# Performance work log

Hardware: AMD Instinct MI355X
Metric: run time of the kernel (lower is better)

The kernel has to match this reference:

```python
import jax, jax.numpy as jnp
import numpy as np
import math

D_MODEL = 2048
NUM_HEADS = 16
D_K = D_MODEL // NUM_HEADS  # 128
THETA = 10000.0
BATCH = 2
SEQ = 2048


def setup_inputs() -> dict:
    key = jax.random.key(0)
    k1, k2, k3 = jax.random.split(key, 3)
    std_qkv = math.sqrt(2.0 / (D_MODEL + 3 * D_MODEL))
    std_o = math.sqrt(2.0 / (D_MODEL + D_MODEL))
    return {
        "x": jax.random.normal(k1, (BATCH, SEQ, D_MODEL), dtype=jnp.float32),
        "token_positions": jnp.arange(SEQ, dtype=jnp.int64 if jax.config.jax_enable_x64 else jnp.int32),
        "Wqkv": jax.random.normal(k2, (3 * D_MODEL, D_MODEL), dtype=jnp.float32) * std_qkv,
        "Wo": jax.random.normal(k3, (D_MODEL, D_MODEL), dtype=jnp.float32) * std_o,
    }


def _rope(x, positions):
    # x: [b, h, t, d_k]; interleaved even/odd rotation as in the torch module
    half = D_K // 2
    inv_freq = 1.0 / (THETA ** (jnp.arange(half, dtype=x.dtype) / half))
    ang = positions.astype(x.dtype)[:, None] * inv_freq[None, :]  # [t, half]
    sin, cos = jnp.sin(ang), jnp.cos(ang)                          # broadcast over b,h
    x_even, x_odd = x[..., 0::2], x[..., 1::2]
    rot_even = x_even * cos - x_odd * sin
    rot_odd = x_even * sin + x_odd * cos
    return jnp.stack([rot_even, rot_odd], axis=-1).reshape(x.shape)


def reference(x, token_positions, Wqkv, Wo):
    B, T, _ = x.shape
    qkv = x @ Wqkv.T                                  # [b, t, 3*d_model]
    q, k, v = jnp.split(qkv, 3, axis=-1)
    def to_heads(t):
        return t.reshape(B, T, NUM_HEADS, D_K).transpose(0, 2, 1, 3)  # b h t d
    q, k, v = to_heads(q), to_heads(k), to_heads(v)
    q = _rope(q, token_positions)
    k = _rope(k, token_positions)
    scale = 1.0 / math.sqrt(D_K)
    scores = jnp.einsum("bhqd,bhkd->bhqk", q, k) * scale
    causal = jnp.tril(jnp.ones((T, T), dtype=bool))
    scores = jnp.where(causal, scores, jnp.finfo(scores.dtype).min)
    attn = jax.nn.softmax(scores, axis=-1)
    out = jnp.einsum("bhqk,bhkd->bhqd", attn, v)
    out = out.transpose(0, 2, 1, 3).reshape(B, T, D_MODEL)
    return out @ Wo.T
```

## Files before the change

### kernel.cpp

```cpp
#include <hip/hip_runtime.h>
#include <math.h>
#include <stdint.h>

#define NHEADS 16
#define DK 128
#define TSEQ 2048
#define DMODEL 2048

typedef __attribute__((ext_vector_type(8))) short short8;
typedef __attribute__((ext_vector_type(4))) float floatx4;

__device__ __forceinline__ float bf2f(unsigned short h) {
    return __uint_as_float(((unsigned int)h) << 16);
}
__device__ __forceinline__ unsigned short f2bf(float f) {
    unsigned int u = __float_as_uint(f);
    u += 0x7FFFu + ((u >> 16) & 1u);
    return (unsigned short)(u >> 16);
}
__device__ __forceinline__ void async16(unsigned short* lds, const unsigned short* g) {
    __builtin_amdgcn_global_load_lds(
        (const __attribute__((address_space(1))) uint32_t*)g,
        (__attribute__((address_space(3))) uint32_t*)lds, 16, 0, 0);
}

#define NX8 1048576
#define NW8 1572864
#define NO8 524288
__global__ __launch_bounds__(256) void cast_all_bf16(
    const float* __restrict__ x, const float* __restrict__ wqkv, const float* __restrict__ wo,
    unsigned short* __restrict__ xb, unsigned short* __restrict__ wqkvb, unsigned short* __restrict__ wob)
{
    const int i = blockIdx.x * 256 + threadIdx.x;
    const float* src; unsigned short* dst; int k;
    if (i < NX8)            { src = x;    dst = xb;    k = i; }
    else if (i < NX8 + NW8) { src = wqkv; dst = wqkvb; k = i - NX8; }
    else                    { src = wo;   dst = wob;   k = i - NX8 - NW8; }
    const float4* p4 = reinterpret_cast<const float4*>(src) + 2 * (size_t)k;
    const float4 a = p4[0], b = p4[1];
    uint32_t w0 = (uint32_t)f2bf(a.x) | ((uint32_t)f2bf(a.y) << 16);
    uint32_t w1 = (uint32_t)f2bf(a.z) | ((uint32_t)f2bf(a.w) << 16);
    uint32_t w2 = (uint32_t)f2bf(b.x) | ((uint32_t)f2bf(b.y) << 16);
    uint32_t w3 = (uint32_t)f2bf(b.z) | ((uint32_t)f2bf(b.w) << 16);
    uint4 o; o.x = w0; o.y = w1; o.z = w2; o.w = w3;
    *reinterpret_cast<uint4*>(dst + 8 * (size_t)k) = o;
}

__global__ __launch_bounds__(256) void rope_table_kernel(
    const int* __restrict__ pos, float2* __restrict__ tab)
{
    const int idx = blockIdx.x * 256 + threadIdx.x;
    const int tt = idx >> 6, i = idx & 63;
    const double inv_freq = exp(-log(10000.0) * (double)i / 64.0);
    const double ang = (double)pos[tt] * inv_freq;
    tab[idx] = make_float2((float)cos(ang), (float)sin(ang));
}

__global__ __launch_bounds__(512, 1) void gemm_qkv_8ph(
    const unsigned short* __restrict__ A, const unsigned short* __restrict__ B,
    unsigned short* __restrict__ qkvb, unsigned short* __restrict__ vt,
    const float2* __restrict__ tab)
{
    const int K = DMODEL, N = 3 * DMODEL;
    __shared__ unsigned short As[2][256 * 64];
    __shared__ unsigned short Bs[2][192 * 64];

    const int t = threadIdx.x;
    const int lane = t & 63, w = t >> 6;
    const int wr = w >> 2, wc = w & 3;
    const int lr = lane & 15, hi = lane >> 4;

    const int bid = (int)blockIdx.x;
    const int xcd = bid & 7, local = bid >> 3;
    const int row0 = (local & 15) * 256;
    const int col0 = ((xcd << 2) | (local >> 4)) * 192;

    const int rr = t >> 3;
    const int cc = ((t & 7) ^ (rr & 7)) << 3;
    const unsigned short* aP = A + (size_t)(row0 + rr) * K + cc;
    const unsigned short* bP = B + (size_t)(col0 + rr) * K + cc;
    const size_t rstep = (size_t)64 * K;

    floatx4 acc[8][3];
#pragma unroll
    for (int m = 0; m < 8; m++)
#pragma unroll
        for (int n = 0; n < 3; n++)
#pragma unroll
            for (int e = 0; e < 4; e++) acc[m][n][e] = 0.f;

#define STAGE_A(nb, k0n) do { \
        async16(&As[nb][t * 8],          aP + (k0n)); \
        async16(&As[nb][(t + 512) * 8],  aP + rstep + (k0n)); \
        async16(&As[nb][(t + 1024) * 8], aP + 2 * rstep + (k0n)); \
        async16(&As[nb][(t + 1536) * 8], aP + 3 * rstep + (k0n)); \
    } while (0)
#define STAGE_B(nb, k0n) do { \
        async16(&Bs[nb][t * 8],          bP + (k0n)); \
        async16(&Bs[nb][(t + 512) * 8],  bP + rstep + (k0n)); \
        async16(&Bs[nb][(t + 1024) * 8], bP + 2 * rstep + (k0n)); \
    } while (0)

    STAGE_A(0, 0);
    STAGE_B(0, 0);
    const int NT = K >> 6;
    const int ch0 = (hi ^ (lr & 7)) * 8;
    const int ch1 = ((4 + hi) ^ (lr & 7)) * 8;

    short8 av[4][2], bv[3][2];

    for (int kt = 0; kt < NT; ++kt) {
        const int cur = kt & 1;
        const unsigned short* __restrict__ Ac = &As[cur][0];
        const unsigned short* __restrict__ Bc = &Bs[cur][0];

        if (kt + 1 < NT) {
            STAGE_A(cur ^ 1, (kt + 1) << 6);
            asm volatile("s_waitcnt vmcnt(4)" ::: "memory");
        } else {
            asm volatile("s_waitcnt vmcnt(0)" ::: "memory");
        }
        __builtin_amdgcn_s_barrier();
        __builtin_amdgcn_sched_barrier(0);

#pragma unroll
        for (int m = 0; m < 4; m++) {
            const int ar = (wr * 128 + m * 16 + lr) * 64;
            av[m][0] = *(const short8*)&Ac[ar + ch0];
            av[m][1] = *(const short8*)&Ac[ar + ch1];
        }
#pragma unroll
        for (int n = 0; n < 3; n++) {
            const int br = (wc * 48 + n * 16 + lr) * 64;
            bv[n][0] = *(const short8*)&Bc[br + ch0];
            bv[n][1] = *(const short8*)&Bc[br + ch1];
        }
        asm volatile("s_waitcnt lgkmcnt(0)" ::: "memory");
        __builtin_amdgcn_sched_barrier(0);
        __builtin_amdgcn_s_setprio(1);
#pragma unroll
        for (int m = 0; m < 4; m++)
#pragma unroll
            for (int n = 0; n < 3; n++) {
                acc[m][n] = __builtin_amdgcn_mfma_f32_16x16x32_bf16(av[m][0], bv[n][0], acc[m][n], 0, 0, 0);
                acc[m][n] = __builtin_amdgcn_mfma_f32_16x16x32_bf16(av[m][1], bv[n][1], acc[m][n], 0, 0, 0);
            }
        __builtin_amdgcn_s_setprio(0);
        __builtin_amdgcn_s_barrier();

        if (kt + 1 < NT) STAGE_B(cur ^ 1, (kt + 1) << 6);
#pragma unroll
        for (int m = 0; m < 4; m++) {
            const int ar = (wr * 128 + 64 + m * 16 + lr) * 64;
            av[m][0] = *(const short8*)&Ac[ar + ch0];
            av[m][1] = *(const short8*)&Ac[ar + ch1];
        }
        __builtin_amdgcn_s_barrier();
        asm volatile("s_waitcnt lgkmcnt(0)" ::: "memory");
        __builtin_amdgcn_sched_barrier(0);
        __builtin_amdgcn_s_setprio(1);
#pragma unroll
        for (int m = 0; m < 4; m++)
#pragma unroll
            for (int n = 0; n < 3; n++) {
                acc[4 + m][n] = __builtin_amdgcn_mfma_f32_16x16x32_bf16(av[m][0], bv[n][0], acc[4 + m][n], 0, 0, 0);
                acc[4 + m][n] = __builtin_amdgcn_mfma_f32_16x16x32_bf16(av[m][1], bv[n][1], acc[4 + m][n], 0, 0, 0);
            }
        __builtin_amdgcn_s_setprio(0);
        __builtin_amdgcn_s_barrier();
    }
#undef STAGE_A
#undef STAGE_B

    const int par = lr & 1;
#pragma unroll
    for (int mi = 0; mi < 8; mi++) {
        const int row = row0 + wr * 128 + mi * 16 + hi * 4;
        const int tt = row & (TSEQ - 1);
        const int bb = row >> 11;
#pragma unroll
        for (int ni = 0; ni < 3; ni++) {
            const int col = col0 + wc * 48 + ni * 16 + lr;
            if (col < 2 * DMODEL) {
                const int pi = (col & 127) >> 1;
#pragma unroll
                for (int j = 0; j < 4; j++) {
                    const float2 cs = tab[(tt + j) * 64 + pi];
                    const float v = acc[mi][ni][j];
                    const float p = __shfl_xor(v, 1, 64);
                    const float o = par ? (p * cs.y + v * cs.x)
                                        : (v * cs.x - p * cs.y);
                    qkvb[(size_t)(row + j) * N + col] = f2bf(o);
                }
            } else {
                const int vcol = col - 2 * DMODEL;
                const int h = vcol >> 7, d = vcol & 127;
                uint2 pw;
                pw.x = (uint32_t)f2bf(acc[mi][ni][0]) | ((uint32_t)f2bf(acc[mi][ni][1]) << 16);
                pw.y = (uint32_t)f2bf(acc[mi][ni][2]) | ((uint32_t)f2bf(acc[mi][ni][3]) << 16);
                *(uint2*)&vt[(size_t)((bb * NHEADS + h) * DK + d) * TSEQ + tt] = pw;
            }
        }
    }
}

__global__ __launch_bounds__(512, 1) void gemm_o_8ph(
    const unsigned short* __restrict__ A, const unsigned short* __restrict__ B,
    float* __restrict__ C)
{
    const int K = DMODEL, N = DMODEL;
    __shared__ unsigned short As[2][256 * 64];
    __shared__ unsigned short Bs[2][128 * 64];

    const int t = threadIdx.x;
    const int lane = t & 63, w = t >> 6;
    const int wr = w >> 2, wc = w & 3;
    const int lr = lane & 15, hi = lane >> 4;

    const int bid = (int)blockIdx.x;
    const int xcd = bid & 7, local = bid >> 3;
    const int row0 = (local & 15) * 256;
    const int col0 = ((xcd << 1) | (local >> 4)) * 128;

    const int rr = t >> 3;
    const int cc = ((t & 7) ^ (rr & 7)) << 3;
    const unsigned short* aP = A + (size_t)(row0 + rr) * K + cc;
    const unsigned short* bP = B + (size_t)(col0 + rr) * K + cc;
    const size_t rstep = (size_t)64 * K;

    floatx4 acc[8][2];
#pragma unroll
    for (int m = 0; m < 8; m++)
#pragma unroll
        for (int n = 0; n < 2; n++)
#pragma unroll
            for (int e = 0; e < 4; e++) acc[m][n][e] = 0.f;

#define STAGE(nb, k0n) do { \
        async16(&As[nb][t * 8],          aP + (k0n)); \
        async16(&As[nb][(t + 512) * 8],  aP + rstep + (k0n)); \
        async16(&As[nb][(t + 1024) * 8], aP + 2 * rstep + (k0n)); \
        async16(&As[nb][(t + 1536) * 8], aP + 3 * rstep + (k0n)); \
        async16(&Bs[nb][t * 8],          bP + (k0n)); \
        async16(&Bs[nb][(t + 512) * 8],  bP + rstep + (k0n)); \
    } while (0)

    STAGE(0, 0);
    const int NT = K >> 6;
    const int ch0 = (hi ^ (lr & 7)) * 8;
    const int ch1 = ((4 + hi) ^ (lr & 7)) * 8;

    short8 av[4][2], bv[2][2];

    for (int kt = 0; kt < NT; ++kt) {
        const int cur = kt & 1;
        const unsigned short* __restrict__ Ac = &As[cur][0];
        const unsigned short* __restrict__ Bc = &Bs[cur][0];

        if (kt + 1 < NT) {
            STAGE(cur ^ 1, (kt + 1) << 6);
            asm volatile("s_waitcnt vmcnt(6)" ::: "memory");
        } else {
            asm volatile("s_waitcnt vmcnt(0)" ::: "memory");
        }
        __builtin_amdgcn_s_barrier();
        __builtin_amdgcn_sched_barrier(0);

#pragma unroll
        for (int m = 0; m < 4; m++) {
            const int ar = (wr * 128 + m * 16 + lr) * 64;
            av[m][0] = *(const short8*)&Ac[ar + ch0];
            av[m][1] = *(const short8*)&Ac[ar + ch1];
        }
#pragma unroll
        for (int n = 0; n < 2; n++) {
            const int br = (wc * 32 + n * 16 + lr) * 64;
            bv[n][0] = *(const short8*)&Bc[br + ch0];
            bv[n][1] = *(const short8*)&Bc[br + ch1];
        }
        asm volatile("s_waitcnt lgkmcnt(0)" ::: "memory");
        __builtin_amdgcn_sched_barrier(0);
        __builtin_amdgcn_s_setprio(1);
#pragma unroll
        for (int m = 0; m < 4; m++)
#pragma unroll
            for (int n = 0; n < 2; n++) {
                acc[m][n] = __builtin_amdgcn_mfma_f32_16x16x32_bf16(av[m][0], bv[n][0], acc[m][n], 0, 0, 0);
                acc[m][n] = __builtin_amdgcn_mfma_f32_16x16x32_bf16(av[m][1], bv[n][1], acc[m][n], 0, 0, 0);
            }
        __builtin_amdgcn_s_setprio(0);
        __builtin_amdgcn_s_barrier();

#pragma unroll
        for (int m = 0; m < 4; m++) {
            const int ar = (wr * 128 + 64 + m * 16 + lr) * 64;
            av[m][0] = *(const short8*)&Ac[ar + ch0];
            av[m][1] = *(const short8*)&Ac[ar + ch1];
        }
        __builtin_amdgcn_s_barrier();
        asm volatile("s_waitcnt lgkmcnt(0)" ::: "memory");
        __builtin_amdgcn_sched_barrier(0);
        __builtin_amdgcn_s_setprio(1);
#pragma unroll
        for (int m = 0; m < 4; m++)
#pragma unroll
            for (int n = 0; n < 2; n++) {
                acc[4 + m][n] = __builtin_amdgcn_mfma_f32_16x16x32_bf16(av[m][0], bv[n][0], acc[4 + m][n], 0, 0, 0);
                acc[4 + m][n] = __builtin_amdgcn_mfma_f32_16x16x32_bf16(av[m][1], bv[n][1], acc[4 + m][n], 0, 0, 0);
            }
        __builtin_amdgcn_s_setprio(0);
        __builtin_amdgcn_s_barrier();
    }
#undef STAGE

#pragma unroll
    for (int mi = 0; mi < 8; mi++) {
        const int row = row0 + wr * 128 + mi * 16 + hi * 4;
#pragma unroll
        for (int ni = 0; ni < 2; ni++) {
            const int col = col0 + wc * 32 + ni * 16 + lr;
#pragma unroll
            for (int j = 0; j < 4; j++)
                C[(size_t)(row + j) * N + col] = acc[mi][ni][j];
        }
    }
}

__global__ __launch_bounds__(256, 2) void attn_mfma2_kernel(
    const unsigned short* __restrict__ qkvb, const unsigned short* __restrict__ vt,
    unsigned short* __restrict__ outb)
{
    __shared__ unsigned short Ks[2][64 * 128];
    __shared__ unsigned short Vs[128 * 64];
    __shared__ unsigned short Ps[4][32 * 64];

    const int t = threadIdx.x;
    const int lane = t & 63, w = t >> 6;
    const int lr = lane & 15, hi = lane >> 4;
    const int bh = blockIdx.y, b = bh >> 4, h = bh & 15;
    const int qc = (int)gridDim.x - 1 - (int)blockIdx.x;
    const int q0 = qc * 128;
    const int q0w = q0 + w * 32;
    const float scale = 0.08838834764831845f;
    const size_t QROW = 3 * DMODEL;

    const unsigned short* kg = qkvb + (size_t)b * TSEQ * QROW + DMODEL + h * DK;
    const unsigned short* vg = vt + (size_t)bh * DK * TSEQ;

    short8 qf[2][4];
    {
        const unsigned short* qbase = qkvb + (size_t)(b * TSEQ + q0w) * QROW + h * DK;
#pragma unroll
        for (int nt = 0; nt < 2; nt++)
#pragma unroll
            for (int ks = 0; ks < 4; ks++) {
                short8 raw = *(const short8*)(qbase + (size_t)(nt * 16 + lr) * QROW + ks * 32 + hi * 8);
                short8 sc;
#pragma unroll
                for (int e = 0; e < 8; e++)
                    sc[e] = (short)f2bf(bf2f((unsigned short)raw[e]) * scale);
                qf[nt][ks] = sc;
            }
    }

    auto stageK = [&](int bufi, int kv0s) {
#pragma unroll
        for (int i = 0; i < 4; i++) {
            const int s = i * 256 + t;
            const int r = s >> 4;
            const int cc = (s & 15) ^ (r & 7);
            async16(&Ks[bufi][s * 8], kg + (size_t)(kv0s + r) * QROW + cc * 8);
        }
    };
    auto stageV = [&](int kv0s) {
#pragma unroll
        for (int i = 0; i < 4; i++) {
            const int s = i * 256 + t;
            const int r = s >> 3;
            const int cc = (s & 7) ^ (r & 7);
            async16(&Vs[s * 8], vg + (size_t)r * TSEQ + kv0s + cc * 8);
        }
    };

    floatx4 accO[2][8];
#pragma unroll
    for (int nt = 0; nt < 2; nt++)
#pragma unroll
        for (int dt = 0; dt < 8; dt++)
#pragma unroll
            for (int e = 0; e < 4; e++) accO[nt][dt][e] = 0.f;
    float mrun[2] = {-1e30f, -1e30f};
    float lrun[2] = {0.f, 0.f};

    const int ntiles = (q0 + 128) / 64;
    int kbuf = 0;

    stageK(0, 0);
    __syncthreads();

    const int pswz = (lr & 7) << 1;

    for (int ti = 0; ti < ntiles; ti++) {
        const int kv0 = ti * 64;
        const bool havK = (ti + 1 < ntiles);
        stageV(kv0);
        if (havK) stageK(kbuf ^ 1, kv0 + 64);

        const bool active = (kv0 <= q0w + 31);
        float al[2] = {1.f, 1.f};

        if (active) {
            floatx4 st[4][2];
#pragma unroll
            for (int mt = 0; mt < 4; mt++)
#pragma unroll
                for (int nt = 0; nt < 2; nt++)
#pragma unroll
                    for (int e = 0; e < 4; e++) st[mt][nt][e] = 0.f;
#pragma unroll
            for (int mt = 0; mt < 4; mt++) {
                const int r = mt * 16 + lr;
#pragma unroll
                for (int ks = 0; ks < 4; ks++) {
                    const int ch = (ks * 4 + hi) ^ (r & 7);
                    const short8 kf = *(const short8*)&Ks[kbuf][(r * 16 + ch) * 8];
                    st[mt][0] = __builtin_amdgcn_mfma_f32_16x16x32_bf16(kf, qf[0][ks], st[mt][0], 0, 0, 0);
                    st[mt][1] = __builtin_amdgcn_mfma_f32_16x16x32_bf16(kf, qf[1][ks], st[mt][1], 0, 0, 0);
                }
            }
            if (kv0 + 63 > q0w) {
#pragma unroll
                for (int nt = 0; nt < 2; nt++) {
                    const int qg = q0w + nt * 16 + lr;
#pragma unroll
                    for (int mt = 0; mt < 4; mt++)
#pragma unroll
                        for (int rg = 0; rg < 4; rg++) {
                            const int kvg = kv0 + mt * 16 + hi * 4 + rg;
                            if (kvg > qg) st[mt][nt][rg] = -1e30f;
                        }
                }
            }
            float pm[2];
#pragma unroll
            for (int nt = 0; nt < 2; nt++) {
                float m = -1e30f;
#pragma unroll
                for (int mt = 0; mt < 4; mt++)
#pragma unroll
                    for (int rg = 0; rg < 4; rg++) m = fmaxf(m, st[mt][nt][rg]);
                m = fmaxf(m, __shfl_xor(m, 16, 64));
                m = fmaxf(m, __shfl_xor(m, 32, 64));
                pm[nt] = m;
            }
            if (__any((pm[0] > mrun[0] + 8.f) || (pm[1] > mrun[1] + 8.f))) {
#pragma unroll
                for (int nt = 0; nt < 2; nt++) {
                    const float mn = fmaxf(mrun[nt], pm[nt]);
                    al[nt] = __expf(mrun[nt] - mn);
                    mrun[nt] = mn;
                }
#pragma unroll
                for (int rg = 0; rg < 4; rg++) {
                    const float a0 = __shfl(al[0], hi * 4 + rg, 64);
                    const float a1 = __shfl(al[1], hi * 4 + rg, 64);
#pragma unroll
                    for (int dt = 0; dt < 8; dt++) {
                        accO[0][dt][rg] *= a0;
                        accO[1][dt][rg] *= a1;
                    }
                }
            }
#pragma unroll
            for (int nt = 0; nt < 2; nt++) {
                float ls = 0.f;
                const int prow = nt * 16 + lr;
#pragma unroll
                for (int mt = 0; mt < 4; mt++) {
                    float pv[4];
#pragma unroll
                    for (int rg = 0; rg < 4; rg++) {
                        pv[rg] = __expf(st[mt][nt][rg] - mrun[nt]);
                        ls += pv[rg];
                    }
                    uint2 pw;
                    pw.x = (uint32_t)f2bf(pv[0]) | ((uint32_t)f2bf(pv[1]) << 16);
                    pw.y = (uint32_t)f2bf(pv[2]) | ((uint32_t)f2bf(pv[3]) << 16);
                    const int chunk = (mt * 4 + hi) ^ pswz;
                    *(uint2*)&Ps[w][prow * 64 + chunk * 4] = pw;
                }
                ls += __shfl_xor(ls, 16, 64);
                ls += __shfl_xor(ls, 32, 64);
                lrun[nt] = lrun[nt] * al[nt] + ls;
            }
        }
        if (havK) asm volatile("s_waitcnt vmcnt(4)" ::: "memory");
        else      asm volatile("s_waitcnt vmcnt(0)" ::: "memory");
        __builtin_amdgcn_s_barrier();

        if (active) {
#pragma unroll
            for (int ks2 = 0; ks2 < 2; ks2++) {
                const int ch0 = ((ks2 * 8 + hi * 2) ^ pswz) * 4;
                const short8 pa0 = *(const short8*)&Ps[w][(0 * 16 + lr) * 64 + ch0];
                const short8 pa1 = *(const short8*)&Ps[w][(1 * 16 + lr) * 64 + ch0];
#pragma unroll
                for (int dt = 0; dt < 8; dt++) {
                    const int r = dt * 16 + lr;
                    const int ch = (ks2 * 4 + hi) ^ (r & 7);
                    const short8 vf = *(const short8*)&Vs[(r * 8 + ch) * 8];
                    accO[0][dt] = __builtin_amdgcn_mfma_f32_16x16x32_bf16(pa0, vf, accO[0][dt], 0, 0, 0);
                    accO[1][dt] = __builtin_amdgcn_mfma_f32_16x16x32_bf16(pa1, vf, accO[1][dt], 0, 0, 0);
                }
            }
        }
        asm volatile("s_waitcnt vmcnt(0)" ::: "memory");
        __builtin_amdgcn_s_barrier();
        kbuf ^= 1;
    }

#pragma unroll
    for (int nt = 0; nt < 2; nt++) {
        const float lv_own = 1.f / lrun[nt];
#pragma unroll
        for (int rg = 0; rg < 4; rg++) {
            const float lv = __shfl(lv_own, hi * 4 + rg, 64);
            unsigned short* orow = outb + (size_t)(b * TSEQ + q0w + nt * 16 + hi * 4 + rg) * DMODEL + h * DK;
#pragma unroll
            for (int dt = 0; dt < 8; dt++)
                orow[dt * 16 + lr] = f2bf(accO[nt][dt][rg] * lv);
        }
    }
}

extern "C" void kernel_launch(void* const* d_in, const int* in_sizes, int n_in,
                              void* d_out, int out_size, void* d_ws, size_t ws_size,
                              hipStream_t stream)
{
    const float* x    = (const float*)d_in[0];
    const int*   pos  = (const int*)d_in[1];
    const float* Wqkv = (const float*)d_in[2];
    const float* Wo   = (const float*)d_in[3];
    float* out = (float*)d_out;

    unsigned short* qkvb  = (unsigned short*)d_ws;
    unsigned short* vtb   = qkvb + (size_t)25165824;
    unsigned short* xb    = vtb + (size_t)8388608;
    unsigned short* attnb = xb;
    unsigned short* wqkvb = xb + (size_t)8388608;
    unsigned short* wob   = wqkvb + (size_t)12582912;
    float2* tab = (float2*)(wob + (size_t)4194304);

    cast_all_bf16<<<12288, 256, 0, stream>>>(x, Wqkv, Wo, xb, wqkvb, wob);
    rope_table_kernel<<<512, 256, 0, stream>>>(pos, tab);

    gemm_qkv_8ph<<<dim3(512), 512, 0, stream>>>(xb, wqkvb, qkvb, vtb, tab);

    attn_mfma2_kernel<<<dim3(16, 32), 256, 0, stream>>>(qkvb, vtb, attnb);

    gemm_o_8ph<<<dim3(256), 512, 0, stream>>>(attnb, wob, out);
}
```

Baseline: 285.8 us.

## Software-pipeline LDS fragment reads in QKV and output GEMMs, cut barriers

Both bf16 MFMA GEMM main loops are restructured so the next tile's first A half and the B fragments are read from LDS at the end of the previous iteration. The second A half is read while the first MFMA batch runs, using separate av0/av1 register sets. This drops the per-iteration barriers from four to one and overlaps LDS reads and global-to-LDS staging with matrix math. The cost is more vector registers for the doubled A fragments and a full vmcnt(0) wait before each barrier, which could hurt occupancy or expose global load latency.

```diff
diff --git a/kernel.cpp b/kernel.cpp
--- a/kernel.cpp
+++ b/kernel.cpp
@@ -101,40 +101,59 @@
         async16(&Bs[nb][(t + 1024) * 8], bP + 2 * rstep + (k0n)); \
     } while (0)
 
-    STAGE_A(0, 0);
-    STAGE_B(0, 0);
     const int NT = K >> 6;
     const int ch0 = (hi ^ (lr & 7)) * 8;
     const int ch1 = ((4 + hi) ^ (lr & 7)) * 8;
 
-    short8 av[4][2], bv[3][2];
+    short8 av0[4][2], av1[4][2], bv[3][2];
+
+#define RD_A(dst, Ac, mh) do { \
+        _Pragma("unroll") \
+        for (int m = 0; m < 4; m++) { \
+            const int ar = (wr * 128 + (mh) * 64 + m * 16 + lr) * 64; \
+            dst[m][0] = *(const short8*)&(Ac)[ar + ch0]; \
+            dst[m][1] = *(const short8*)&(Ac)[ar + ch1]; \
+        } \
+    } while (0)
+#define RD_B(Bc) do { \
+        _Pragma("unroll") \
+        for (int n = 0; n < 3; n++) { \
+            const int br = (wc * 48 + n * 16 + lr) * 64; \
+            bv[n][0] = *(const short8*)&(Bc)[br + ch0]; \
+            bv[n][1] = *(const short8*)&(Bc)[br + ch1]; \
+        } \
+    } while (0)
+
+    STAGE_A(0, 0);
+    STAGE_B(0, 0);
+    asm volatile("s_waitcnt vmcnt(0)" ::: "memory");
+    __builtin_amdgcn_s_barrier();
+    RD_A(av0, &As[0][0], 0);
+    RD_B(&Bs[0][0]);
 
     for (int kt = 0; kt < NT; ++kt) {
         const int cur = kt & 1;
         const unsigned short* __restrict__ Ac = &As[cur][0];
         const unsigned short* __restrict__ Bc = &Bs[cur][0];
-
-        if (kt + 1 < NT) {
-            STAGE_A(cur ^ 1, (kt + 1) << 6);
-            asm volatile("s_waitcnt vmcnt(4)" ::: "memory");
-        } else {
-            asm volatile("s_waitcnt vmcnt(0)" ::: "memory");
-        }
-        __builtin_amdgcn_s_barrier();
+        const unsigned short* __restrict__ An = &As[cur ^ 1][0];
+        const unsigned short* __restrict__ Bn = &Bs[cur ^ 1][0];
+        const bool more = (kt + 1 < NT);
+
+        if (more) STAGE_A(cur ^ 1, (kt + 1) << 6);
+        RD_A(av1, Ac, 1);
+        asm volatile("s_waitcnt lgkmcnt(8)" ::: "memory");
         __builtin_amdgcn_sched_barrier(0);
-
-#pragma unroll
-        for (int m = 0; m < 4; m++) {
-            const int ar = (wr * 128 + m * 16 + lr) * 64;
-            av[m][0] = *(const short8*)&Ac[ar + ch0];
-            av[m][1] = *(const short8*)&Ac[ar + ch1];
-        }
-#pragma unroll
-        for (int n = 0; n < 3; n++) {
-            const int br = (wc * 48 + n * 16 + lr) * 64;
-            bv[n][0] = *(const short8*)&Bc[br + ch0];
-            bv[n][1] = *(const short8*)&Bc[br + ch1];
-        }
+        __builtin_amdgcn_s_setprio(1);
+#pragma unroll
+        for (int m = 0; m < 4; m++)
+#pragma unroll
+            for (int n = 0; n < 3; n++) {
+                acc[m][n] = __builtin_amdgcn_mfma_f32_16x16x32_bf16(av0[m][0], bv[n][0], acc[m][n], 0, 0, 0);
+                acc[m][n] = __builtin_amdgcn_mfma_f32_16x16x32_bf16(av0[m][1], bv[n][1], acc[m][n], 0, 0, 0);
+            }
+        __builtin_amdgcn_s_setprio(0);
+
+        if (more) STAGE_B(cur ^ 1, (kt + 1) << 6);
         asm volatile("s_waitcnt lgkmcnt(0)" ::: "memory");
         __builtin_amdgcn_sched_barrier(0);
         __builtin_amdgcn_s_setprio(1);
@@ -142,35 +161,22 @@
         for (int m = 0; m < 4; m++)
 #pragma unroll
             for (int n = 0; n < 3; n++) {
-                acc[m][n] = __builtin_amdgcn_mfma_f32_16x16x32_bf16(av[m][0], bv[n][0], acc[m][n], 0, 0, 0);
-                acc[m][n] = __builtin_amdgcn_mfma_f32_16x16x32_bf16(av[m][1], bv[n][1], acc[m][n], 0, 0, 0);
+                acc[4 + m][n] = __builtin_amdgcn_mfma_f32_16x16x32_bf16(av1[m][0], bv[n][0], acc[4 + m][n], 0, 0, 0);
+                acc[4 + m][n] = __builtin_amdgcn_mfma_f32_16x16x32_bf16(av1[m][1], bv[n][1], acc[4 + m][n], 0, 0, 0);
             }
         __builtin_amdgcn_s_setprio(0);
-        __builtin_amdgcn_s_barrier();
-
-        if (kt + 1 < NT) STAGE_B(cur ^ 1, (kt + 1) << 6);
-#pragma unroll
-        for (int m = 0; m < 4; m++) {
-            const int ar = (wr * 128 + 64 + m * 16 + lr) * 64;
-            av[m][0] = *(const short8*)&Ac[ar + ch0];
-            av[m][1] = *(const short8*)&Ac[ar + ch1];
-        }
-        __builtin_amdgcn_s_barrier();
-        asm volatile("s_waitcnt lgkmcnt(0)" ::: "memory");
-        __builtin_amdgcn_sched_barrier(0);
-        __builtin_amdgcn_s_setprio(1);
-#pragma unroll
-        for (int m = 0; m < 4; m++)
-#pragma unroll
-            for (int n = 0; n < 3; n++) {
-                acc[4 + m][n] = __builtin_amdgcn_mfma_f32_16x16x32_bf16(av[m][0], bv[n][0], acc[4 + m][n], 0, 0, 0);
-                acc[4 + m][n] = __builtin_amdgcn_mfma_f32_16x16x32_bf16(av[m][1], bv[n][1], acc[4 + m][n], 0, 0, 0);
-            }
-        __builtin_amdgcn_s_setprio(0);
-        __builtin_amdgcn_s_barrier();
+
+        if (more) {
+            asm volatile("s_waitcnt vmcnt(0)" ::: "memory");
+            __builtin_amdgcn_s_barrier();
+            RD_A(av0, An, 0);
+            RD_B(Bn);
+        }
     }
 #undef STAGE_A
 #undef STAGE_B
+#undef RD_A
+#undef RD_B
 
     const int par = lr & 1;
 #pragma unroll
@@ -236,48 +242,69 @@
 #pragma unroll
             for (int e = 0; e < 4; e++) acc[m][n][e] = 0.f;
 
-#define STAGE(nb, k0n) do { \
+#define STAGE_A(nb, k0n) do { \
         async16(&As[nb][t * 8],          aP + (k0n)); \
         async16(&As[nb][(t + 512) * 8],  aP + rstep + (k0n)); \
         async16(&As[nb][(t + 1024) * 8], aP + 2 * rstep + (k0n)); \
         async16(&As[nb][(t + 1536) * 8], aP + 3 * rstep + (k0n)); \
+    } while (0)
+#define STAGE_B(nb, k0n) do { \
         async16(&Bs[nb][t * 8],          bP + (k0n)); \
         async16(&Bs[nb][(t + 512) * 8],  bP + rstep + (k0n)); \
     } while (0)
 
-    STAGE(0, 0);
     const int NT = K >> 6;
     const int ch0 = (hi ^ (lr & 7)) * 8;
     const int ch1 = ((4 + hi) ^ (lr & 7)) * 8;
 
-    short8 av[4][2], bv[2][2];
+    short8 av0[4][2], av1[4][2], bv[2][2];
+
+#define RD_A(dst, Ac, mh) do { \
+        _Pragma("unroll") \
+        for (int m = 0; m < 4; m++) { \
+            const int ar = (wr * 128 + (mh) * 64 + m * 16 + lr) * 64; \
+            dst[m][0] = *(const short8*)&(Ac)[ar + ch0]; \
+            dst[m][1] = *(const short8*)&(Ac)[ar + ch1]; \
+        } \
+    } while (0)
+#define RD_B(Bc) do { \
+        _Pragma("unroll") \
+        for (int n = 0; n < 2; n++) { \
+            const int br = (wc * 32 + n * 16 + lr) * 64; \
+            bv[n][0] = *(const short8*)&(Bc)[br + ch0]; \
+            bv[n][1] = *(const short8*)&(Bc)[br + ch1]; \
+        } \
+    } while (0)
+
+    STAGE_A(0, 0);
+    STAGE_B(0, 0);
+    asm volatile("s_waitcnt vmcnt(0)" ::: "memory");
+    __builtin_amdgcn_s_barrier();
+    RD_A(av0, &As[0][0], 0);
+    RD_B(&Bs[0][0]);
 
     for (int kt = 0; kt < NT; ++kt) {
         const int cur = kt & 1;
         const unsigned short* __restrict__ Ac = &As[cur][0];
-        const unsigned short* __restrict__ Bc = &Bs[cur][0];
-
-        if (kt + 1 < NT) {
-            STAGE(cur ^ 1, (kt + 1) << 6);
-            asm volatile("s_waitcnt vmcnt(6)" ::: "memory");
-        } else {
-            asm volatile("s_waitcnt vmcnt(0)" ::: "memory");
-        }
-        __builtin_amdgcn_s_barrier();
+        const unsigned short* __restrict__ An = &As[cur ^ 1][0];
+        const unsigned short* __restrict__ Bn = &Bs[cur ^ 1][0];
+        const bool more = (kt + 1 < NT);
+
+        if (more) STAGE_A(cur ^ 1, (kt + 1) << 6);
+        RD_A(av1, Ac, 1);
+        asm volatile("s_waitcnt lgkmcnt(8)" ::: "memory");
         __builtin_amdgcn_sched_barrier(0);
-
-#pragma unroll
-        for (int m = 0; m < 4; m++) {
-            const int ar = (wr * 128 + m * 16 + lr) * 64;
-            av[m][0] = *(const short8*)&Ac[ar + ch0];
-            av[m][1] = *(const short8*)&Ac[ar + ch1];
-        }
-#pragma unroll
-        for (int n = 0; n < 2; n++) {
-            const int br = (wc * 32 + n * 16 + lr) * 64;
-            bv[n][0] = *(const short8*)&Bc[br + ch0];
-            bv[n][1] = *(const short8*)&Bc[br + ch1];
-        }
+        __builtin_amdgcn_s_setprio(1);
+#pragma unroll
+        for (int m = 0; m < 4; m++)
+#pragma unroll
+            for (int n = 0; n < 2; n++) {
+                acc[m][n] = __builtin_amdgcn_mfma_f32_16x16x32_bf16(av0[m][0], bv[n][0], acc[m][n], 0, 0, 0);
+                acc[m][n] = __builtin_amdgcn_mfma_f32_16x16x32_bf16(av0[m][1], bv[n][1], acc[m][n], 0, 0, 0);
+            }
+        __builtin_amdgcn_s_setprio(0);
+
+        if (more) STAGE_B(cur ^ 1, (kt + 1) << 6);
         asm volatile("s_waitcnt lgkmcnt(0)" ::: "memory");
         __builtin_amdgcn_sched_barrier(0);
         __builtin_amdgcn_s_setprio(1);
@@ -285,33 +312,22 @@
         for (int m = 0; m < 4; m++)
 #pragma unroll
             for (int n = 0; n < 2; n++) {
-                acc[m][n] = __builtin_amdgcn_mfma_f32_16x16x32_bf16(av[m][0], bv[n][0], acc[m][n], 0, 0, 0);
-                acc[m][n] = __builtin_amdgcn_mfma_f32_16x16x32_bf16(av[m][1], bv[n][1], acc[m][n], 0, 0, 0);
+                acc[4 + m][n] = __builtin_amdgcn_mfma_f32_16x16x32_bf16(av1[m][0], bv[n][0], acc[4 + m][n], 0, 0, 0);
+                acc[4 + m][n] = __builtin_amdgcn_mfma_f32_16x16x32_bf16(av1[m][1], bv[n][1], acc[4 + m][n], 0, 0, 0);
             }
         __builtin_amdgcn_s_setprio(0);
-        __builtin_amdgcn_s_barrier();
-
-#pragma unroll
-        for (int m = 0; m < 4; m++) {
-            const int ar = (wr * 128 + 64 + m * 16 + lr) * 64;
-            av[m][0] = *(const short8*)&Ac[ar + ch0];
-            av[m][1] = *(const short8*)&Ac[ar + ch1];
-        }
-        __builtin_amdgcn_s_barrier();
-        asm volatile("s_waitcnt lgkmcnt(0)" ::: "memory");
-        __builtin_amdgcn_sched_barrier(0);
-        __builtin_amdgcn_s_setprio(1);
-#pragma unroll
-        for (int m = 0; m < 4; m++)
-#pragma unroll
-            for (int n = 0; n < 2; n++) {
-                acc[4 + m][n] = __builtin_amdgcn_mfma_f32_16x16x32_bf16(av[m][0], bv[n][0], acc[4 + m][n], 0, 0, 0);
-                acc[4 + m][n] = __builtin_amdgcn_mfma_f32_16x16x32_bf16(av[m][1], bv[n][1], acc[4 + m][n], 0, 0, 0);
-            }
-        __builtin_amdgcn_s_setprio(0);
-        __builtin_amdgcn_s_barrier();
-    }
-#undef STAGE
+
+        if (more) {
+            asm volatile("s_waitcnt vmcnt(0)" ::: "memory");
+            __builtin_amdgcn_s_barrier();
+            RD_A(av0, An, 0);
+            RD_B(Bn);
+        }
+    }
+#undef STAGE_A
+#undef STAGE_B
+#undef RD_A
+#undef RD_B
 
 #pragma unroll
     for (int mi = 0; mi < 8; mi++) {
```

Result: no change. 285.9 us (+0.1%).

## Retile QKV and output GEMMs to 128-row blocks, 256 threads, two blocks per CU

Applied to the files above, without the earlier changes.

Both projection GEMMs move from 512-thread blocks with 256-row tiles and one block per CU to 256-thread blocks with 128-row tiles, launch bounds of two blocks per CU, and twice as many blocks. Each warp now covers a 64-row by wider-column sub-tile, and the k-step is split into two halves of the 64-wide slab instead of two row halves. A and B staging is merged into a single prefetch with one barrier per iteration. The goal is higher occupancy and less intra-block synchronisation, at the cost of lower per-block operand reuse and more total global/LDS traffic.

```diff
diff --git a/kernel.cpp b/kernel.cpp
--- a/kernel.cpp
+++ b/kernel.cpp
@@ -56,131 +56,122 @@
     tab[idx] = make_float2((float)cos(ang), (float)sin(ang));
 }
 
-__global__ __launch_bounds__(512, 1) void gemm_qkv_8ph(
+__global__ __launch_bounds__(256, 2) void gemm_qkv_x(
     const unsigned short* __restrict__ A, const unsigned short* __restrict__ B,
     unsigned short* __restrict__ qkvb, unsigned short* __restrict__ vt,
     const float2* __restrict__ tab)
 {
     const int K = DMODEL, N = 3 * DMODEL;
-    __shared__ unsigned short As[2][256 * 64];
+    __shared__ unsigned short As[2][128 * 64];
     __shared__ unsigned short Bs[2][192 * 64];
 
     const int t = threadIdx.x;
     const int lane = t & 63, w = t >> 6;
-    const int wr = w >> 2, wc = w & 3;
+    const int wr = w >> 1, wc = w & 1;
     const int lr = lane & 15, hi = lane >> 4;
 
     const int bid = (int)blockIdx.x;
     const int xcd = bid & 7, local = bid >> 3;
-    const int row0 = (local & 15) * 256;
-    const int col0 = ((xcd << 2) | (local >> 4)) * 192;
+    const int row0 = (local & 31) * 128;
+    const int col0 = ((xcd << 2) | (local >> 5)) * 192;
 
     const int rr = t >> 3;
     const int cc = ((t & 7) ^ (rr & 7)) << 3;
     const unsigned short* aP = A + (size_t)(row0 + rr) * K + cc;
     const unsigned short* bP = B + (size_t)(col0 + rr) * K + cc;
-    const size_t rstep = (size_t)64 * K;
-
-    floatx4 acc[8][3];
-#pragma unroll
-    for (int m = 0; m < 8; m++)
-#pragma unroll
-        for (int n = 0; n < 3; n++)
+    const size_t rstep = (size_t)32 * K;
+
+    floatx4 acc[4][6];
+#pragma unroll
+    for (int m = 0; m < 4; m++)
+#pragma unroll
+        for (int n = 0; n < 6; n++)
 #pragma unroll
             for (int e = 0; e < 4; e++) acc[m][n][e] = 0.f;
 
-#define STAGE_A(nb, k0n) do { \
+#define STAGE(nb, k0n) do { \
         async16(&As[nb][t * 8],          aP + (k0n)); \
-        async16(&As[nb][(t + 512) * 8],  aP + rstep + (k0n)); \
-        async16(&As[nb][(t + 1024) * 8], aP + 2 * rstep + (k0n)); \
-        async16(&As[nb][(t + 1536) * 8], aP + 3 * rstep + (k0n)); \
-    } while (0)
-#define STAGE_B(nb, k0n) do { \
+        async16(&As[nb][(t + 256) * 8],  aP + rstep + (k0n)); \
+        async16(&As[nb][(t + 512) * 8],  aP + 2 * rstep + (k0n)); \
+        async16(&As[nb][(t + 768) * 8],  aP + 3 * rstep + (k0n)); \
         async16(&Bs[nb][t * 8],          bP + (k0n)); \
-        async16(&Bs[nb][(t + 512) * 8],  bP + rstep + (k0n)); \
-        async16(&Bs[nb][(t + 1024) * 8], bP + 2 * rstep + (k0n)); \
-    } while (0)
-
-    STAGE_A(0, 0);
-    STAGE_B(0, 0);
+        async16(&Bs[nb][(t + 256) * 8],  bP + rstep + (k0n)); \
+        async16(&Bs[nb][(t + 512) * 8],  bP + 2 * rstep + (k0n)); \
+        async16(&Bs[nb][(t + 768) * 8],  bP + 3 * rstep + (k0n)); \
+        async16(&Bs[nb][(t + 1024) * 8], bP + 4 * rstep + (k0n)); \
+        async16(&Bs[nb][(t + 1280) * 8], bP + 5 * rstep + (k0n)); \
+    } while (0)
+
     const int NT = K >> 6;
     const int ch0 = (hi ^ (lr & 7)) * 8;
     const int ch1 = ((4 + hi) ^ (lr & 7)) * 8;
 
-    short8 av[4][2], bv[3][2];
+    short8 av[4], bv[6];
+
+#define RD_AV(Ac, ch) do { \
+        _Pragma("unroll") \
+        for (int m = 0; m < 4; m++) \
+            av[m] = *(const short8*)&(Ac)[(wr * 64 + m * 16 + lr) * 64 + (ch)]; \
+    } while (0)
+#define RD_BV(Bc, ch) do { \
+        _Pragma("unroll") \
+        for (int n = 0; n < 6; n++) \
+            bv[n] = *(const short8*)&(Bc)[(wc * 96 + n * 16 + lr) * 64 + (ch)]; \
+    } while (0)
+#define MFMA_ALL() do { \
+        _Pragma("unroll") \
+        for (int m = 0; m < 4; m++) \
+            _Pragma("unroll") \
+            for (int n = 0; n < 6; n++) \
+                acc[m][n] = __builtin_amdgcn_mfma_f32_16x16x32_bf16(av[m], bv[n], acc[m][n], 0, 0, 0); \
+    } while (0)
+
+    STAGE(0, 0);
 
     for (int kt = 0; kt < NT; ++kt) {
         const int cur = kt & 1;
         const unsigned short* __restrict__ Ac = &As[cur][0];
         const unsigned short* __restrict__ Bc = &Bs[cur][0];
-
-        if (kt + 1 < NT) {
-            STAGE_A(cur ^ 1, (kt + 1) << 6);
-            asm volatile("s_waitcnt vmcnt(4)" ::: "memory");
+        const bool more = (kt + 1 < NT);
+
+        if (more) {
+            STAGE(cur ^ 1, (kt + 1) << 6);
+            asm volatile("s_waitcnt vmcnt(10)" ::: "memory");
         } else {
             asm volatile("s_waitcnt vmcnt(0)" ::: "memory");
         }
         __builtin_amdgcn_s_barrier();
-        __builtin_amdgcn_sched_barrier(0);
-
-#pragma unroll
-        for (int m = 0; m < 4; m++) {
-            const int ar = (wr * 128 + m * 16 + lr) * 64;
-            av[m][0] = *(const short8*)&Ac[ar + ch0];
-            av[m][1] = *(const short8*)&Ac[ar + ch1];
-        }
-#pragma unroll
-        for (int n = 0; n < 3; n++) {
-            const int br = (wc * 48 + n * 16 + lr) * 64;
-            bv[n][0] = *(const short8*)&Bc[br + ch0];
-            bv[n][1] = *(const short8*)&Bc[br + ch1];
-        }
+
+        RD_AV(Ac, ch0); RD_BV(Bc, ch0);
         asm volatile("s_waitcnt lgkmcnt(0)" ::: "memory");
         __builtin_amdgcn_sched_barrier(0);
         __builtin_amdgcn_s_setprio(1);
-#pragma unroll
-        for (int m = 0; m < 4; m++)
-#pragma unroll
-            for (int n = 0; n < 3; n++) {
-                acc[m][n] = __builtin_amdgcn_mfma_f32_16x16x32_bf16(av[m][0], bv[n][0], acc[m][n], 0, 0, 0);
-                acc[m][n] = __builtin_amdgcn_mfma_f32_16x16x32_bf16(av[m][1], bv[n][1], acc[m][n], 0, 0, 0);
-            }
+        MFMA_ALL();
         __builtin_amdgcn_s_setprio(0);
-        __builtin_amdgcn_s_barrier();
-
-        if (kt + 1 < NT) STAGE_B(cur ^ 1, (kt + 1) << 6);
-#pragma unroll
-        for (int m = 0; m < 4; m++) {
-            const int ar = (wr * 128 + 64 + m * 16 + lr) * 64;
-            av[m][0] = *(const short8*)&Ac[ar + ch0];
-            av[m][1] = *(const short8*)&Ac[ar + ch1];
-        }
-        __builtin_amdgcn_s_barrier();
+
+        RD_AV(Ac, ch1); RD_BV(Bc, ch1);
         asm volatile("s_waitcnt lgkmcnt(0)" ::: "memory");
         __builtin_amdgcn_sched_barrier(0);
         __builtin_amdgcn_s_setprio(1);
-#pragma unroll
-        for (int m = 0; m < 4; m++)
-#pragma unroll
-            for (int n = 0; n < 3; n++) {
-                acc[4 + m][n] = __builtin_amdgcn_mfma_f32_16x16x32_bf16(av[m][0], bv[n][0], acc[4 + m][n], 0, 0, 0);
-                acc[4 + m][n] = __builtin_amdgcn_mfma_f32_16x16x32_bf16(av[m][1], bv[n][1], acc[4 + m][n], 0, 0, 0);
-            }
+        MFMA_ALL();
         __builtin_amdgcn_s_setprio(0);
+
         __builtin_amdgcn_s_barrier();
     }
-#undef STAGE_A
-#undef STAGE_B
+#undef STAGE
+#undef RD_AV
+#undef RD_BV
+#undef MFMA_ALL
 
     const int par = lr & 1;
 #pragma unroll
-    for (int mi = 0; mi < 8; mi++) {
-        const int row = row0 + wr * 128 + mi * 16 + hi * 4;
+    for (int mi = 0; mi < 4; mi++) {
+        const int row = row0 + wr * 64 + mi * 16 + hi * 4;
         const int tt = row & (TSEQ - 1);
         const int bb = row >> 11;
 #pragma unroll
-        for (int ni = 0; ni < 3; ni++) {
-            const int col = col0 + wc * 48 + ni * 16 + lr;
+        for (int ni = 0; ni < 6; ni++) {
+            const int col = col0 + wc * 96 + ni * 16 + lr;
             if (col < 2 * DMODEL) {
                 const int pi = (col & 127) >> 1;
 #pragma unroll
@@ -204,121 +195,116 @@
     }
 }
 
-__global__ __launch_bounds__(512, 1) void gemm_o_8ph(
+__global__ __launch_bounds__(256, 2) void gemm_o_x(
     const unsigned short* __restrict__ A, const unsigned short* __restrict__ B,
     float* __restrict__ C)
 {
     const int K = DMODEL, N = DMODEL;
-    __shared__ unsigned short As[2][256 * 64];
+    __shared__ unsigned short As[2][128 * 64];
     __shared__ unsigned short Bs[2][128 * 64];
 
     const int t = threadIdx.x;
     const int lane = t & 63, w = t >> 6;
-    const int wr = w >> 2, wc = w & 3;
+    const int wr = w >> 1, wc = w & 1;
     const int lr = lane & 15, hi = lane >> 4;
 
     const int bid = (int)blockIdx.x;
     const int xcd = bid & 7, local = bid >> 3;
-    const int row0 = (local & 15) * 256;
-    const int col0 = ((xcd << 1) | (local >> 4)) * 128;
+    const int row0 = (local & 31) * 128;
+    const int col0 = ((xcd << 1) | (local >> 5)) * 128;
 
     const int rr = t >> 3;
     const int cc = ((t & 7) ^ (rr & 7)) << 3;
     const unsigned short* aP = A + (size_t)(row0 + rr) * K + cc;
     const unsigned short* bP = B + (size_t)(col0 + rr) * K + cc;
-    const size_t rstep = (size_t)64 * K;
-
-    floatx4 acc[8][2];
-#pragma unroll
-    for (int m = 0; m < 8; m++)
-#pragma unroll
-        for (int n = 0; n < 2; n++)
+    const size_t rstep = (size_t)32 * K;
+
+    floatx4 acc[4][4];
+#pragma unroll
+    for (int m = 0; m < 4; m++)
+#pragma unroll
+        for (int n = 0; n < 4; n++)
 #pragma unroll
             for (int e = 0; e < 4; e++) acc[m][n][e] = 0.f;
 
 #define STAGE(nb, k0n) do { \
         async16(&As[nb][t * 8],          aP + (k0n)); \
-        async16(&As[nb][(t + 512) * 8],  aP + rstep + (k0n)); \
-        async16(&As[nb][(t + 1024) * 8], aP + 2 * rstep + (k0n)); \
-        async16(&As[nb][(t + 1536) * 8], aP + 3 * rstep + (k0n)); \
+        async16(&As[nb][(t + 256) * 8],  aP + rstep + (k0n)); \
+        async16(&As[nb][(t + 512) * 8],  aP + 2 * rstep + (k0n)); \
+        async16(&As[nb][(t + 768) * 8],  aP + 3 * rstep + (k0n)); \
         async16(&Bs[nb][t * 8],          bP + (k0n)); \
-        async16(&Bs[nb][(t + 512) * 8],  bP + rstep + (k0n)); \
-    } while (0)
-
-    STAGE(0, 0);
+        async16(&Bs[nb][(t + 256) * 8],  bP + rstep + (k0n)); \
+        async16(&Bs[nb][(t + 512) * 8],  bP + 2 * rstep + (k0n)); \
+        async16(&Bs[nb][(t + 768) * 8],  bP + 3 * rstep + (k0n)); \
+    } while (0)
+
     const int NT = K >> 6;
     const int ch0 = (hi ^ (lr & 7)) * 8;
     const int ch1 = ((4 + hi) ^ (lr & 7)) * 8;
 
-    short8 av[4][2], bv[2][2];
+    short8 av[4], bv[4];
+
+#define RD_AV(Ac, ch) do { \
+        _Pragma("unroll") \
+        for (int m = 0; m < 4; m++) \
+            av[m] = *(const short8*)&(Ac)[(wr * 64 + m * 16 + lr) * 64 + (ch)]; \
+    } while (0)
+#define RD_BV(Bc, ch) do { \
+        _Pragma("unroll") \
+        for (int n = 0; n < 4; n++) \
+            bv[n] = *(const short8*)&(Bc)[(wc * 64 + n * 16 + lr) * 64 + (ch)]; \
+    } while (0)
+#define MFMA_ALL() do { \
+        _Pragma("unroll") \
+        for (int m = 0; m < 4; m++) \
+            _Pragma("unroll") \
+            for (int n = 0; n < 4; n++) \
+                acc[m][n] = __builtin_amdgcn_mfma_f32_16x16x32_bf16(av[m], bv[n], acc[m][n], 0, 0, 0); \
+    } while (0)
+
+    STAGE(0, 0);
 
     for (int kt = 0; kt < NT; ++kt) {
         const int cur = kt & 1;
         const unsigned short* __restrict__ Ac = &As[cur][0];
         const unsigned short* __restrict__ Bc = &Bs[cur][0];
-
-        if (kt + 1 < NT) {
+        const bool more = (kt + 1 < NT);
+
+        if (more) {
             STAGE(cur ^ 1, (kt + 1) << 6);
-            asm volatile("s_waitcnt vmcnt(6)" ::: "memory");
+            asm volatile("s_waitcnt vmcnt(8)" ::: "memory");
         } else {
             asm volatile("s_waitcnt vmcnt(0)" ::: "memory");
         }
         __builtin_amdgcn_s_barrier();
-        __builtin_amdgcn_sched_barrier(0);
-
-#pragma unroll
-        for (int m = 0; m < 4; m++) {
-            const int ar = (wr * 128 + m * 16 + lr) * 64;
-            av[m][0] = *(const short8*)&Ac[ar + ch0];
-            av[m][1] = *(const short8*)&Ac[ar + ch1];
-        }
-#pragma unroll
-        for (int n = 0; n < 2; n++) {
-            const int br = (wc * 32 + n * 16 + lr) * 64;
-            bv[n][0] = *(const short8*)&Bc[br + ch0];
-            bv[n][1] = *(const short8*)&Bc[br + ch1];
-        }
+
+        RD_AV(Ac, ch0); RD_BV(Bc, ch0);
         asm volatile("s_waitcnt lgkmcnt(0)" ::: "memory");
         __builtin_amdgcn_sched_barrier(0);
         __builtin_amdgcn_s_setprio(1);
-#pragma unroll
-        for (int m = 0; m < 4; m++)
-#pragma unroll
-            for (int n = 0; n < 2; n++) {
-                acc[m][n] = __builtin_amdgcn_mfma_f32_16x16x32_bf16(av[m][0], bv[n][0], acc[m][n], 0, 0, 0);
-                acc[m][n] = __builtin_amdgcn_mfma_f32_16x16x32_bf16(av[m][1], bv[n][1], acc[m][n], 0, 0, 0);
-            }
+        MFMA_ALL();
         __builtin_amdgcn_s_setprio(0);
-        __builtin_amdgcn_s_barrier();
-
-#pragma unroll
-        for (int m = 0; m < 4; m++) {
-            const int ar = (wr * 128 + 64 + m * 16 + lr) * 64;
-            av[m][0] = *(const short8*)&Ac[ar + ch0];
-            av[m][1] = *(const short8*)&Ac[ar + ch1];
-        }
-        __builtin_amdgcn_s_barrier();
+
+        RD_AV(Ac, ch1); RD_BV(Bc, ch1);
         asm volatile("s_waitcnt lgkmcnt(0)" ::: "memory");
         __builtin_amdgcn_sched_barrier(0);
         __builtin_amdgcn_s_setprio(1);
-#pragma unroll
-        for (int m = 0; m < 4; m++)
-#pragma unroll
-            for (int n = 0; n < 2; n++) {
-                acc[4 + m][n] = __builtin_amdgcn_mfma_f32_16x16x32_bf16(av[m][0], bv[n][0], acc[4 + m][n], 0, 0, 0);
-                acc[4 + m][n] = __builtin_amdgcn_mfma_f32_16x16x32_bf16(av[m][1], bv[n][1], acc[4 + m][n], 0, 0, 0);
-            }
+        MFMA_ALL();
         __builtin_amdgcn_s_setprio(0);
+
         __builtin_amdgcn_s_barrier();
     }
 #undef STAGE
-
-#pragma unroll
-    for (int mi = 0; mi < 8; mi++) {
-        const int row = row0 + wr * 128 + mi * 16 + hi * 4;
-#pragma unroll
-        for (int ni = 0; ni < 2; ni++) {
-            const int col = col0 + wc * 32 + ni * 16 + lr;
+#undef RD_AV
+#undef RD_BV
+#undef MFMA_ALL
+
+#pragma unroll
+    for (int mi = 0; mi < 4; mi++) {
+        const int row = row0 + wr * 64 + mi * 16 + hi * 4;
+#pragma unroll
+        for (int ni = 0; ni < 4; ni++) {
+            const int col = col0 + wc * 64 + ni * 16 + lr;
 #pragma unroll
             for (int j = 0; j < 4; j++)
                 C[(size_t)(row + j) * N + col] = acc[mi][ni][j];
@@ -554,9 +540,9 @@
     cast_all_bf16<<<12288, 256, 0, stream>>>(x, Wqkv, Wo, xb, wqkvb, wob);
     rope_table_kernel<<<512, 256, 0, stream>>>(pos, tab);
 
-    gemm_qkv_8ph<<<dim3(512), 512, 0, stream>>>(xb, wqkvb, qkvb, vtb, tab);
+    gemm_qkv_x<<<dim3(1024), 256, 0, stream>>>(xb, wqkvb, qkvb, vtb, tab);
 
     attn_mfma2_kernel<<<dim3(16, 32), 256, 0, stream>>>(qkvb, vtb, attnb);
 
-    gemm_o_8ph<<<dim3(256), 512, 0, stream>>>(attnb, wob, out);
-}
+    gemm_o_x<<<dim3(512), 256, 0, stream>>>(attnb, wob, out);
+}
```

Measured after the change: 266.6 us. -6.7%, faster.
